# Kernel optimization log

Measured on AMD Instinct MI355X. Metric: run time of the kernel, lower is better.

Reference implementation:

```python
import jax, jax.numpy as jnp
import numpy as np

DR = 0.1
L = 24.0
N_FRAMES = 16
N_ATOMS = 512


def setup_inputs() -> dict:
    key = jax.random.key(0)
    # coordinates uniform in the periodic box [0, L)^3
    traj = jax.random.uniform(key, (N_FRAMES, N_ATOMS, 3), dtype=jnp.float32) * L
    cell = jnp.eye(3, dtype=jnp.float32) * L
    # r_list = arange(0.5*dr, L_max - 2*dr, dr) with L_max = cell[0,0]/2 -> 118 bins
    r_list = jnp.arange(0.5 * DR, L / 2 - 2 * DR, DR, dtype=jnp.float32)
    return {"traj": traj, "cell": cell, "r_list": r_list}


def _frame_hist(q, cell_diag, r_list, cutoff_sq):
    # q: [N,3]; dense minimum-image pairwise displacements, upper-triangle pairs only
    disp = q[None, :, :] - q[:, None, :]                        # [N,N,3]
    offsets = jax.lax.stop_gradient(jnp.floor(disp / cell_diag + 0.5))
    disp = disp - offsets * cell_diag                           # minimum image
    sq = jnp.sum(disp * disp, axis=-1)                          # [N,N]
    n = q.shape[0]
    triu = jnp.triu(jnp.ones((n, n), dtype=bool))               # torch.triu zeros lower part
    sq = jnp.where(triu, sq, 0.0)
    mask = (sq < cutoff_sq) & (sq != 0.0)                       # i<j and within cutoff
    d = jnp.sqrt(jnp.where(mask, sq, 1.0))                      # safe sqrt (masked out below)
    centered = d[:, :, None] - r_list[None, None, :]            # [N,N,B]
    g = (1.0 / (DR * np.sqrt(2.0 * np.pi))) * jnp.exp(-0.5 * (centered / DR) ** 2)
    g = g * mask[:, :, None].astype(g.dtype)                    # drop excluded pairs (== nonzero extraction)
    return g.sum(axis=(0, 1)) * DR                              # [B]


def reference(traj, cell, r_list):
    cell_diag = jnp.diag(cell)                                  # [3]
    cutoff_sq = (cell[0, 0] / 2.0) ** 2                         # L_max = cell[0,0]/2 (default)

    def step(acc, q):
        return acc + _frame_hist(q, cell_diag, r_list, cutoff_sq), None

    hist0 = jnp.zeros(r_list.shape, dtype=traj.dtype)
    hist, _ = jax.lax.scan(step, hist0, traj)                   # accumulate over frames like the python loop
    hist = hist / traj.shape[0]

    v = (4.0 * np.pi / 3.0) * ((r_list + 0.5 * DR) ** 3 - (r_list - 0.5 * DR) ** 3)
    natom = traj.shape[1]
    det = jnp.linalg.det(cell)
    gr = hist / v * det / (natom - 1) / natom * 2.0
    return (r_list, gr)
```

## Files before the change

### kernel.cpp

```cpp
#include <hip/hip_runtime.h>
#include <math.h>

#define N_ATOMS 512
#define MAX_B 128
#define NBUCK 64
#define WIN 0.45f

__global__ void zero_kernel(float* p, int n) {
    int t = blockIdx.x * blockDim.x + threadIdx.x;
    if (t < n) p[t] = 0.0f;
}

__global__ __launch_bounds__(256) void pair_kernel(
    const float* __restrict__ traj, const float* __restrict__ cell,
    const float* __restrict__ r_list, float* __restrict__ part,
    int B, int atomic_mode)
{
    __shared__ float2 qxy[N_ATOMS];
    __shared__ float  qzs[N_ATOMS];
    __shared__ float  dsorted[2048];
    __shared__ int    cnt[NBUCK];
    __shared__ int    start[NBUCK + 1];
    __shared__ int    cursor[NBUCK];
    __shared__ float  accbuf[256];

    const int frame = blockIdx.x >> 6;
    const int sub   = blockIdx.x & 63;
    const int tid   = threadIdx.x;

    const float* q = traj + (size_t)frame * (N_ATOMS * 3);
    for (int a = tid; a < N_ATOMS; a += 256) {
        qxy[a] = make_float2(q[3 * a + 0], q[3 * a + 1]);
        qzs[a] = q[3 * a + 2];
    }
    if (tid < NBUCK) cnt[tid] = 0;
    __syncthreads();

    const float L = cell[0];
    const float invL = 1.0f / L;
    const float cutoff_sq = 0.25f * L * L;
    const float inv_bw = (float)NBUCK / (0.5f * L);

    float dval[8];
    int   dbuck[8];
    #pragma unroll
    for (int s = 0; s < 8; ++s) {
        const int qidx = s * 256 + tid;
        const int rp   = sub * 4 + (qidx >> 9);
        const int qq   = qidx & 511;
        const int lenA = 511 - rp;
        const bool inA = qq < lenA;
        const int i = inA ? rp : (510 - rp);
        const int j = inA ? (rp + 1 + qq) : qq;
        const bool vp = !(rp == 255 && !inA);

        const float2 pj = qxy[j];
        const float2 pi = qxy[i];
        float dx = pj.x - pi.x;
        float dy = pj.y - pi.y;
        float dz = qzs[j] - qzs[i];
        dx -= L * floorf(dx * invL + 0.5f);
        dy -= L * floorf(dy * invL + 0.5f);
        dz -= L * floorf(dz * invL + 0.5f);
        const float d2 = dx * dx + dy * dy + dz * dz;

        dbuck[s] = -1;
        dval[s]  = 0.0f;
        if (vp && d2 < cutoff_sq && d2 != 0.0f) {
            const float d = sqrtf(d2);
            int b = (int)(d * inv_bw);
            if (b > NBUCK - 1) b = NBUCK - 1;
            dval[s]  = d;
            dbuck[s] = b;
            atomicAdd(&cnt[b], 1);
        }
    }
    __syncthreads();

    if (tid < NBUCK) {
        const int v = cnt[tid];
        int incl = v;
        #pragma unroll
        for (int off = 1; off < NBUCK; off <<= 1) {
            const int n = __shfl_up(incl, off, 64);
            if (tid >= off) incl += n;
        }
        start[tid + 1] = incl;
        cursor[tid] = incl - v;
        if (tid == 0) start[0] = 0;
    }
    __syncthreads();

    #pragma unroll
    for (int s = 0; s < 8; ++s) {
        if (dbuck[s] >= 0) {
            const int pos = atomicAdd(&cursor[dbuck[s]], 1);
            dsorted[pos] = dval[s];
        }
    }
    __syncthreads();

    const int k = tid & 127;
    const int g = tid >> 7;
    float acc = 0.0f;
    if (k < B) {
        const float rk = r_list[k];
        const float c1 = -50.0f;
        const float c2 = 100.0f * rk;
        const float c3 = -50.0f * rk * rk;
        int blo = (int)(fmaxf((rk - WIN) * inv_bw, 0.0f));
        int bhi = (int)((rk + WIN) * inv_bw);
        if (bhi > NBUCK - 1) bhi = NBUCK - 1;
        const int lo = start[blo];
        const int hi = start[bhi + 1];
        int idx = lo + g;
        int nn = hi - idx;
        nn = (nn > 0) ? ((nn + 1) >> 1) : 0;
        float acc1 = 0.0f;
        int m = nn >> 1;
        while (m-- > 0) {
            const float d0 = dsorted[idx];
            const float d1 = dsorted[idx + 2];
            idx += 4;
            acc  += __expf(fmaf(d0, fmaf(c1, d0, c2), c3));
            acc1 += __expf(fmaf(d1, fmaf(c1, d1, c2), c3));
        }
        if (nn & 1) {
            const float d0 = dsorted[idx];
            acc += __expf(fmaf(d0, fmaf(c1, d0, c2), c3));
        }
        acc += acc1;
    }
    accbuf[tid] = acc;
    __syncthreads();

    if (tid < 128) {
        const float v = accbuf[tid] + accbuf[tid + 128];
        if (atomic_mode) atomicAdd(&part[(blockIdx.x & 15) * MAX_B + tid], v);
        else             part[(size_t)blockIdx.x * MAX_B + tid] = v;
    }
}

__global__ __launch_bounds__(256) void finalize_kernel(
    const float* __restrict__ r_list, const float* __restrict__ cell,
    const float* __restrict__ part, float* __restrict__ out,
    int B, int F, int nrows)
{
    __shared__ float red[256];
    const int k = blockIdx.x;
    if (k >= B) return;

    float s = 0.0f;
    for (int t = threadIdx.x; t < nrows; t += 256) s += part[(size_t)t * MAX_B + k];
    red[threadIdx.x] = s;
    __syncthreads();
    for (int off = 128; off > 0; off >>= 1) {
        if (threadIdx.x < off) red[threadIdx.x] += red[threadIdx.x + off];
        __syncthreads();
    }
    if (threadIdx.x == 0) {
        const float r = r_list[k];
        out[k] = r;
        const float det = cell[0] * cell[4] * cell[8];
        const float rp = r + 0.05f;
        const float rm = r - 0.05f;
        const float v = (4.0f * (float)M_PI / 3.0f) * (rp * rp * rp - rm * rm * rm);
        const float inv_sqrt2pi = 0.3989422804014327f;
        const float h = red[0] * inv_sqrt2pi / (float)F;
        const float gr = h / v * det / (float)(N_ATOMS - 1) / (float)N_ATOMS * 2.0f;
        out[B + k] = gr;
    }
}

extern "C" void kernel_launch(void* const* d_in, const int* in_sizes, int n_in,
                              void* d_out, int out_size, void* d_ws, size_t ws_size,
                              hipStream_t stream) {
    const float* traj   = (const float*)d_in[0];
    const float* cell   = (const float*)d_in[1];
    const float* r_list = (const float*)d_in[2];
    float* out  = (float*)d_out;
    float* part = (float*)d_ws;

    const int B = in_sizes[2];
    const int F = in_sizes[0] / (N_ATOMS * 3);
    const int nblocks = F * 64;

    const bool partials_fit =
        ws_size >= (size_t)nblocks * MAX_B * sizeof(float);

    if (partials_fit) {
        hipLaunchKernelGGL(pair_kernel, dim3(nblocks), dim3(256), 0, stream,
                           traj, cell, r_list, part, B, 0);
        hipLaunchKernelGGL(finalize_kernel, dim3(MAX_B), dim3(256), 0, stream,
                           r_list, cell, part, out, B, F, nblocks);
    } else {
        hipLaunchKernelGGL(zero_kernel, dim3(8), dim3(256), 0, stream,
                           part, 16 * MAX_B);
        hipLaunchKernelGGL(pair_kernel, dim3(nblocks), dim3(256), 0, stream,
                           traj, cell, r_list, part, B, 1);
        hipLaunchKernelGGL(finalize_kernel, dim3(MAX_B), dim3(256), 0, stream,
                           r_list, cell, part, out, B, F, 16);
    }
}
```

Before: 70.00 us.

## Load-balance Gaussian evaluation across threads via prefix-sum work partitioning

Replaces the fixed per-bin thread assignment with a flattened work list: per-bin pair counts are prefix-summed, and every thread takes an equal slice of the total (bin, distance) work, locating its starting bin by binary search and flushing partial sums with shared-memory atomics. The bucket count is doubled and the Gaussian window narrowed so fewer distances are evaluated per bin. The warp-shuffle bucket scan becomes a shared-memory scan with many barriers, which adds synchronization overhead. The narrower window truncates more of each Gaussian tail, a small accuracy risk.

```diff
diff --git a/kernel.cpp b/kernel.cpp
--- a/kernel.cpp
+++ b/kernel.cpp
@@ -3,8 +3,8 @@
 
 #define N_ATOMS 512
 #define MAX_B 128
-#define NBUCK 64
-#define WIN 0.45f
+#define NBUCK 128
+#define WIN 0.35f
 
 __global__ void zero_kernel(float* p, int n) {
     int t = blockIdx.x * blockDim.x + threadIdx.x;
@@ -22,7 +22,11 @@
     __shared__ int    cnt[NBUCK];
     __shared__ int    start[NBUCK + 1];
     __shared__ int    cursor[NBUCK];
-    __shared__ float  accbuf[256];
+    __shared__ int    scan[128];
+    __shared__ int    Pf[MAX_B + 1];
+    __shared__ int    lobuf[MAX_B];
+    __shared__ float  c2buf[MAX_B], c3buf[MAX_B];
+    __shared__ float  hbuf[MAX_B];
 
     const int frame = blockIdx.x >> 6;
     const int sub   = blockIdx.x & 63;
@@ -77,18 +81,21 @@
     }
     __syncthreads();
 
+    if (tid < NBUCK) scan[tid] = cnt[tid];
+    __syncthreads();
+    #pragma unroll
+    for (int off = 1; off < NBUCK; off <<= 1) {
+        int v = 0;
+        if (tid < NBUCK) { v = scan[tid]; if (tid >= off) v += scan[tid - off]; }
+        __syncthreads();
+        if (tid < NBUCK) scan[tid] = v;
+        __syncthreads();
+    }
     if (tid < NBUCK) {
-        const int v = cnt[tid];
-        int incl = v;
-        #pragma unroll
-        for (int off = 1; off < NBUCK; off <<= 1) {
-            const int n = __shfl_up(incl, off, 64);
-            if (tid >= off) incl += n;
-        }
-        start[tid + 1] = incl;
-        cursor[tid] = incl - v;
-        if (tid == 0) start[0] = 0;
-    }
+        start[tid + 1] = scan[tid];
+        cursor[tid]    = scan[tid] - cnt[tid];
+    }
+    if (tid == 0) start[0] = 0;
     __syncthreads();
 
     #pragma unroll
@@ -98,44 +105,83 @@
             dsorted[pos] = dval[s];
         }
     }
-    __syncthreads();
-
-    const int k = tid & 127;
-    const int g = tid >> 7;
-    float acc = 0.0f;
-    if (k < B) {
-        const float rk = r_list[k];
-        const float c1 = -50.0f;
-        const float c2 = 100.0f * rk;
-        const float c3 = -50.0f * rk * rk;
-        int blo = (int)(fmaxf((rk - WIN) * inv_bw, 0.0f));
-        int bhi = (int)((rk + WIN) * inv_bw);
-        if (bhi > NBUCK - 1) bhi = NBUCK - 1;
-        const int lo = start[blo];
-        const int hi = start[bhi + 1];
-        int idx = lo + g;
-        int nn = hi - idx;
-        nn = (nn > 0) ? ((nn + 1) >> 1) : 0;
-        float acc1 = 0.0f;
-        int m = nn >> 1;
-        while (m-- > 0) {
-            const float d0 = dsorted[idx];
-            const float d1 = dsorted[idx + 2];
-            idx += 4;
-            acc  += __expf(fmaf(d0, fmaf(c1, d0, c2), c3));
-            acc1 += __expf(fmaf(d1, fmaf(c1, d1, c2), c3));
-        }
-        if (nn & 1) {
-            const float d0 = dsorted[idx];
-            acc += __expf(fmaf(d0, fmaf(c1, d0, c2), c3));
-        }
-        acc += acc1;
-    }
-    accbuf[tid] = acc;
-    __syncthreads();
-
-    if (tid < 128) {
-        const float v = accbuf[tid] + accbuf[tid + 128];
+
+    if (tid < MAX_B) {
+        int t = 0, lo = 0;
+        float c2v = 0.0f, c3v = 0.0f;
+        if (tid < B) {
+            const float rk = r_list[tid];
+            c2v = 100.0f * rk;
+            c3v = -50.0f * rk * rk;
+        }
+        lobuf[tid] = 0;
+        c2buf[tid] = c2v;
+        c3buf[tid] = c3v;
+        hbuf[tid]  = 0.0f;
+        scan[tid]  = t;
+        (void)lo;
+    }
+    __syncthreads();
+    if (tid < MAX_B) {
+        int t = 0, lo = 0;
+        if (tid < B) {
+            const float rk = r_list[tid];
+            int blo = (int)(fmaxf((rk - WIN) * inv_bw, 0.0f));
+            int bhi = (int)((rk + WIN) * inv_bw);
+            if (bhi > NBUCK - 1) bhi = NBUCK - 1;
+            lo = start[blo];
+            t  = start[bhi + 1] - lo;
+        }
+        lobuf[tid] = lo;
+        scan[tid]  = t;
+    }
+    __syncthreads();
+    #pragma unroll
+    for (int off = 1; off < MAX_B; off <<= 1) {
+        int v = 0;
+        if (tid < MAX_B) { v = scan[tid]; if (tid >= off) v += scan[tid - off]; }
+        __syncthreads();
+        if (tid < MAX_B) scan[tid] = v;
+        __syncthreads();
+    }
+    if (tid < MAX_B) Pf[tid + 1] = scan[tid];
+    if (tid == 0) Pf[0] = 0;
+    __syncthreads();
+
+    const int W = Pf[MAX_B];
+    const int s0 = (tid * W) >> 8;
+    const int e0 = ((tid + 1) * W) >> 8;
+    if (s0 < e0) {
+        int lo2 = 0, hi2 = MAX_B;
+        #pragma unroll
+        for (int it = 0; it < 7; ++it) {
+            const int mid = (lo2 + hi2) >> 1;
+            if (Pf[mid] <= s0) lo2 = mid; else hi2 = mid;
+        }
+        int   kb   = lo2;
+        int   didx = lobuf[kb] + (s0 - Pf[kb]);
+        int   pend = Pf[kb + 1];
+        float c2   = c2buf[kb];
+        float c3   = c3buf[kb];
+        float acc  = 0.0f;
+        for (int f = s0; f < e0; ++f) {
+            while (f >= pend) {
+                if (acc != 0.0f) { atomicAdd(&hbuf[kb], acc); acc = 0.0f; }
+                ++kb;
+                pend = Pf[kb + 1];
+                didx = lobuf[kb];
+                c2   = c2buf[kb];
+                c3   = c3buf[kb];
+            }
+            const float d = dsorted[didx++];
+            acc += __expf(fmaf(d, fmaf(-50.0f, d, c2), c3));
+        }
+        if (acc != 0.0f) atomicAdd(&hbuf[kb], acc);
+    }
+    __syncthreads();
+
+    if (tid < MAX_B) {
+        const float v = hbuf[tid];
         if (atomic_mode) atomicAdd(&part[(blockIdx.x & 15) * MAX_B + tid], v);
         else             part[(size_t)blockIdx.x * MAX_B + tid] = v;
     }
```

Result: slower. 76.25 us (+8.9%).

## Split histogram bins across 32-lane groups and refine distance buckets

Applied to the files above, without the earlier changes.

Switches the gaussian accumulation from one thread per bin (two threads striding a bin's window) to a 32-lane group per bin. Each group strides the sorted distances in its window and reduces with xor shuffles. Bucket count doubles to 128 and the window narrows to 0.40, so each bin scans fewer candidate distances. The prefix scan now handles two buckets per lane. r_list is staged into shared memory. This is meant to fix load imbalance and serialized per-thread loops, at the cost of more shuffle reductions and a bins-per-group loop.

```diff
diff --git a/kernel.cpp b/kernel.cpp
--- a/kernel.cpp
+++ b/kernel.cpp
@@ -3,8 +3,8 @@
 
 #define N_ATOMS 512
 #define MAX_B 128
-#define NBUCK 64
-#define WIN 0.45f
+#define NBUCK 128
+#define WIN 0.40f
 
 __global__ void zero_kernel(float* p, int n) {
     int t = blockIdx.x * blockDim.x + threadIdx.x;
@@ -22,7 +22,8 @@
     __shared__ int    cnt[NBUCK];
     __shared__ int    start[NBUCK + 1];
     __shared__ int    cursor[NBUCK];
-    __shared__ float  accbuf[256];
+    __shared__ float  rbuf[MAX_B];
+    __shared__ float  hbuf[MAX_B];
 
     const int frame = blockIdx.x >> 6;
     const int sub   = blockIdx.x & 63;
@@ -34,6 +35,10 @@
         qzs[a] = q[3 * a + 2];
     }
     if (tid < NBUCK) cnt[tid] = 0;
+    if (tid < MAX_B) {
+        hbuf[tid] = 0.0f;
+        rbuf[tid] = (tid < B) ? r_list[tid] : 0.0f;
+    }
     __syncthreads();
 
     const float L = cell[0];
@@ -77,16 +82,20 @@
     }
     __syncthreads();
 
-    if (tid < NBUCK) {
-        const int v = cnt[tid];
-        int incl = v;
+    if (tid < 64) {
+        const int c0 = cnt[2 * tid];
+        const int c1 = cnt[2 * tid + 1];
+        const int p  = c0 + c1;
+        int incl = p;
         #pragma unroll
-        for (int off = 1; off < NBUCK; off <<= 1) {
+        for (int off = 1; off < 64; off <<= 1) {
             const int n = __shfl_up(incl, off, 64);
             if (tid >= off) incl += n;
         }
-        start[tid + 1] = incl;
-        cursor[tid] = incl - v;
+        start[2 * tid + 2]  = incl;
+        start[2 * tid + 1]  = incl - c1;
+        cursor[2 * tid]     = incl - p;
+        cursor[2 * tid + 1] = incl - c1;
         if (tid == 0) start[0] = 0;
     }
     __syncthreads();
@@ -100,42 +109,39 @@
     }
     __syncthreads();
 
-    const int k = tid & 127;
-    const int g = tid >> 7;
-    float acc = 0.0f;
-    if (k < B) {
-        const float rk = r_list[k];
-        const float c1 = -50.0f;
+    const int hw   = tid >> 5;
+    const int lane = tid & 31;
+    for (int k = hw; k < B; k += 8) {
+        const float rk = rbuf[k];
         const float c2 = 100.0f * rk;
         const float c3 = -50.0f * rk * rk;
         int blo = (int)(fmaxf((rk - WIN) * inv_bw, 0.0f));
         int bhi = (int)((rk + WIN) * inv_bw);
         if (bhi > NBUCK - 1) bhi = NBUCK - 1;
-        const int lo = start[blo];
         const int hi = start[bhi + 1];
-        int idx = lo + g;
-        int nn = hi - idx;
-        nn = (nn > 0) ? ((nn + 1) >> 1) : 0;
-        float acc1 = 0.0f;
-        int m = nn >> 1;
-        while (m-- > 0) {
+        int idx = start[blo] + lane;
+        float acc0 = 0.0f, acc1 = 0.0f;
+        while (idx + 32 < hi) {
             const float d0 = dsorted[idx];
-            const float d1 = dsorted[idx + 2];
-            idx += 4;
-            acc  += __expf(fmaf(d0, fmaf(c1, d0, c2), c3));
-            acc1 += __expf(fmaf(d1, fmaf(c1, d1, c2), c3));
-        }
-        if (nn & 1) {
+            const float d1 = dsorted[idx + 32];
+            idx += 64;
+            acc0 += __expf(fmaf(d0, fmaf(-50.0f, d0, c2), c3));
+            acc1 += __expf(fmaf(d1, fmaf(-50.0f, d1, c2), c3));
+        }
+        if (idx < hi) {
             const float d0 = dsorted[idx];
-            acc += __expf(fmaf(d0, fmaf(c1, d0, c2), c3));
-        }
-        acc += acc1;
-    }
-    accbuf[tid] = acc;
-    __syncthreads();
-
-    if (tid < 128) {
-        const float v = accbuf[tid] + accbuf[tid + 128];
+            acc0 += __expf(fmaf(d0, fmaf(-50.0f, d0, c2), c3));
+        }
+        float acc = acc0 + acc1;
+        #pragma unroll
+        for (int off = 16; off > 0; off >>= 1)
+            acc += __shfl_xor(acc, off, 32);
+        if (lane == 0) hbuf[k] = acc;
+    }
+    __syncthreads();
+
+    if (tid < MAX_B) {
+        const float v = hbuf[tid];
         if (atomic_mode) atomicAdd(&part[(blockIdx.x & 15) * MAX_B + tid], v);
         else             part[(size_t)blockIdx.x * MAX_B + tid] = v;
     }
```

Result: slower. 73.55 us (+5.1%).
